# Performance work log

Hardware: AMD Instinct MI355X
Metric: run time of the kernel (lower is better)

## Reference

```python
import jax, jax.numpy as jnp
import numpy as np

NUM_HEADS = 16
HEAD_DIM = 128  # embedding_size 2048 / 16 heads
ROPE_BASE = 10000.0


def rope_tables(seq_len, head_dim):
    # matches precompute_rope_params with freq_config=None
    inv_freq = 1.0 / (ROPE_BASE ** (jnp.arange(0, head_dim, 2, dtype=jnp.float32) / head_dim))
    pos = jnp.arange(seq_len, dtype=jnp.float32)
    ang = pos[:, None] * inv_freq[None, :]          # [S, D/2]
    ang = jnp.concatenate([ang, ang], axis=1)        # [S, D]
    return jnp.cos(ang), jnp.sin(ang)


def apply_rope(x, cos, sin):
    # x: [B, H, S, D]
    d = x.shape[-1]
    x1, x2 = x[..., : d // 2], x[..., d // 2:]
    rotated = jnp.concatenate([-x2, x1], axis=-1)
    return x * cos[None, None] + rotated * sin[None, None]


def setup_inputs() -> dict:
    key = jax.random.key(0)
    ks = jax.random.split(key, 5)
    B, S, H = 2, 2048, 2048
    w_scale = 1.0 / np.sqrt(H)  # keep activations sane
    return {
        "x": jax.random.normal(ks[0], (B, S, H), dtype=jnp.float32),
        "Wq": jax.random.normal(ks[1], (H, H), dtype=jnp.float32) * w_scale,
        "Wk": jax.random.normal(ks[2], (H, H), dtype=jnp.float32) * w_scale,
        "Wv": jax.random.normal(ks[3], (H, H), dtype=jnp.float32) * w_scale,
        "Wo": jax.random.normal(ks[4], (H, H), dtype=jnp.float32) * w_scale,
    }


def reference(x, Wq, Wk, Wv, Wo):
    B, S, H = x.shape
    nH, D = NUM_HEADS, HEAD_DIM
    # torch Linear(bias=False): y = x @ W.T
    q = (x @ Wq.T).reshape(B, S, nH, D).transpose(0, 2, 1, 3)  # [B,H,S,D]
    k = (x @ Wk.T).reshape(B, S, nH, D).transpose(0, 2, 1, 3)
    v = (x @ Wv.T).reshape(B, S, nH, D).transpose(0, 2, 1, 3)
    cos, sin = rope_tables(S, D)
    q = apply_rope(q, cos, sin)
    k = apply_rope(k, cos, sin)  # note: v is NOT rotated, matching source
    # Faithful to source bug: scores / (1/sqrt(d)) == scores * sqrt(d)
    scale = jnp.sqrt(jnp.asarray(D, dtype=x.dtype))
    scores = jnp.einsum("bhqd,bhkd->bhqk", q, k) * scale
    causal = jnp.triu(jnp.ones((S, S), dtype=bool), k=1)
    scores = jnp.where(causal[None, None], -jnp.inf, scores)
    attn = jax.nn.softmax(scores, axis=-1)
    ctx = jnp.einsum("bhqk,bhkd->bhqd", attn, v)
    ctx = ctx.transpose(0, 2, 1, 3).reshape(B, S, H)
    return ctx @ Wo.T
```

## Files before the change

kernel.cpp:

```cpp
#include <hip/hip_runtime.h>
#include <cmath>


typedef unsigned short u16;
typedef __attribute__((ext_vector_type(4))) float  f32x4;
typedef __attribute__((ext_vector_type(16))) float f32x16;
typedef __attribute__((ext_vector_type(4))) float  float4v;
typedef __attribute__((ext_vector_type(4))) unsigned short u16x4;
typedef __attribute__((ext_vector_type(8))) unsigned short u16x8;
typedef __attribute__((ext_vector_type(8))) short s16x8;

__device__ __forceinline__ u16 f2bf(float f) {
  unsigned u = __float_as_uint(f);
  u += 0x7FFFu + ((u >> 16) & 1u);
  return (u16)(u >> 16);
}
__device__ __forceinline__ float bf2f(u16 h) {
  return __uint_as_float(((unsigned)h) << 16);
}
__device__ __forceinline__ f32x4 MFMA(s16x8 a, s16x8 b, f32x4 c) {
  return __builtin_amdgcn_mfma_f32_16x16x32_bf16(a, b, c, 0, 0, 0);
}
__device__ __forceinline__ f32x16 MFMA32(s16x8 a, s16x8 b, f32x16 c) {
  return __builtin_amdgcn_mfma_f32_32x32x16_bf16(a, b, c, 0, 0, 0);
}
__device__ __forceinline__ unsigned cvtpk_bf16(float lo, float hi) {
  unsigned r;
  asm("v_cvt_pk_bf16_f32 %0, %1, %2" : "=v"(r) : "v"(lo), "v"(hi));
  return r;
}
__device__ __forceinline__ void gld16(const void* g, void* s) {
  __builtin_amdgcn_global_load_lds(
      (const __attribute__((address_space(1))) void*)g,
      (__attribute__((address_space(3))) void*)s, 16, 0, 0);
}

__global__ void split_bf16(const float* __restrict__ src, u16* __restrict__ hi,
                           u16* __restrict__ lo, int n4) {
  int i = blockIdx.x * 256 + threadIdx.x;
  if (i >= n4) return;
  float4v v = ((const float4v*)src)[i];
  u16x4 hv, lv;
#pragma unroll
  for (int j = 0; j < 4; ++j) {
    float f = v[j];
    u16 h = f2bf(f);
    hv[j] = h;
    lv[j] = f2bf(f - bf2f(h));
  }
  ((u16x4*)hi)[i] = hv;
  if (lo) ((u16x4*)lo)[i] = lv;
}

__global__ void rope_tab(float* __restrict__ cosT, float* __restrict__ sinT) {
  int idx = blockIdx.x * 256 + threadIdx.x;
  int i = idx & 63, s = idx >> 6;
  double invf = pow(10000.0, -(double)i / 64.0);
  double ang = (double)s * invf;
  cosT[idx] = (float)cos(ang);
  sinT[idx] = (float)sin(ang);
}

template <int NTERM, int OMODE, int ROPE>
__global__ __launch_bounds__(256, 3)
void gemm_bt(const u16* __restrict__ Ah, const u16* __restrict__ Al,
             const u16* __restrict__ Bh, const u16* __restrict__ Bl,
             float* __restrict__ Cf, u16* __restrict__ Ch, u16* __restrict__ Cl,
             const float* __restrict__ cosT, const float* __restrict__ sinT,
             float scale, int M, int N, int K) {
  __shared__ u16 As[128 * 32];
  __shared__ u16 Bs[128 * 32];
  __shared__ u16 Asl[NTERM == 3 ? 128 * 32 : 8];
  __shared__ u16 Bsl[NTERM == 3 ? 128 * 32 : 8];
  const int bn = blockIdx.x, bm = blockIdx.y;
  const int t = threadIdx.x;
  const int w = t >> 6, lane = t & 63, quad = lane >> 4, lc = lane & 15;

  const f32x4 ZERO = {0.f, 0.f, 0.f, 0.f};
  f32x4 acc[2][8];
#pragma unroll
  for (int i = 0; i < 2; ++i)
#pragma unroll
    for (int j = 0; j < 8; ++j) acc[i][j] = ZERO;

  const int sr0 = (lane >> 2);
  const int sc0 = (lane & 3) * 8;
  const size_t arow0 = (size_t)bm * 128, brow0 = (size_t)bn * 128;

  for (int k0 = 0; k0 < K; k0 += 32) {
#pragma unroll
    for (int p = 0; p < 2; ++p) {
      const int ch = 2 * w + p;
      const int r = ch * 16 + sr0;
      const size_t ga = (arow0 + r) * (size_t)K + k0 + sc0;
      const size_t gb = (brow0 + r) * (size_t)K + k0 + sc0;
      const int ldso = ch * 512 + lane * 8;
      gld16(&Ah[ga], &As[ldso]);
      gld16(&Bh[gb], &Bs[ldso]);
      if constexpr (NTERM == 3) {
        gld16(&Al[ga], &Asl[ldso]);
        gld16(&Bl[gb], &Bsl[ldso]);
      }
    }
    __syncthreads();

    s16x8 ah[2], al[2];
#pragma unroll
    for (int i = 0; i < 2; ++i) {
      ah[i] = *(const s16x8*)&As[(32 * w + 16 * i + lc) * 32 + 8 * quad];
      if constexpr (NTERM == 3)
        al[i] = *(const s16x8*)&Asl[(32 * w + 16 * i + lc) * 32 + 8 * quad];
    }
#pragma unroll
    for (int j = 0; j < 8; ++j) {
      const s16x8 bh = *(const s16x8*)&Bs[(16 * j + lc) * 32 + 8 * quad];
      s16x8 bl;
      if constexpr (NTERM == 3)
        bl = *(const s16x8*)&Bsl[(16 * j + lc) * 32 + 8 * quad];
#pragma unroll
      for (int i = 0; i < 2; ++i) {
        acc[i][j] = MFMA(ah[i], bh, acc[i][j]);
        if constexpr (NTERM == 3) {
          acc[i][j] = MFMA(ah[i], bl, acc[i][j]);
          acc[i][j] = MFMA(al[i], bh, acc[i][j]);
        }
      }
    }
    __syncthreads();
  }

  if constexpr (ROPE) {
#pragma unroll
    for (int i = 0; i < 2; ++i)
#pragma unroll
      for (int r = 0; r < 4; ++r) {
        const int row = bm * 128 + 32 * w + 16 * i + 4 * quad + r;
        const int s = row & 2047;
#pragma unroll
        for (int j = 0; j < 4; ++j) {
          const int hd = 16 * j + lc;
          const float cs = cosT[s * 64 + hd], sn = sinT[s * 64 + hd];
          const float q1 = acc[i][j][r], q2 = acc[i][j + 4][r];
          const float o1 = (q1 * cs - q2 * sn) * scale;
          const float o2 = (q2 * cs + q1 * sn) * scale;
          const size_t p1 = (size_t)row * N + bn * 128 + hd;
          const u16 h1 = f2bf(o1);
          Ch[p1] = h1; Cl[p1] = f2bf(o1 - bf2f(h1));
          const u16 h2 = f2bf(o2);
          Ch[p1 + 64] = h2; Cl[p1 + 64] = f2bf(o2 - bf2f(h2));
        }
      }
  } else {
#pragma unroll
    for (int i = 0; i < 2; ++i)
#pragma unroll
      for (int j = 0; j < 8; ++j) {
        const int col = bn * 128 + 16 * j + lc;
#pragma unroll
        for (int r = 0; r < 4; ++r) {
          const int row = bm * 128 + 32 * w + 16 * i + 4 * quad + r;
          const float v = acc[i][j][r];
          if constexpr (OMODE == 0) {
            Cf[(size_t)row * N + col] = v;
          } else if constexpr (OMODE == 1) {
            const u16 hv = f2bf(v);
            Ch[(size_t)row * N + col] = hv;
            Cl[(size_t)row * N + col] = f2bf(v - bf2f(hv));
          } else {
            Ch[(size_t)row * N + col] = f2bf(v);
          }
        }
      }
  }
}

__global__ __launch_bounds__(512, 2)
void attn(const u16* __restrict__ Qh, const u16* __restrict__ Ql,
          const u16* __restrict__ Kh, const u16* __restrict__ Kl,
          const u16* __restrict__ Vt, u16* __restrict__ Ctx) {
  __shared__ u16 SMEM[65536];

  const int t = threadIdx.x;
  const int w = t >> 6, lane = t & 63;
  const int l31 = lane & 31, hi = lane >> 5;
  const int swz = (l31 & 7) << 3;
  const int j = w >> 1, kh = w & 1;

  const int bid = (int)blockIdx.x + 8 * (int)blockIdx.y + 128 * (int)blockIdx.z;
  const int xcd = bid & 7, slot = bid >> 3;
  const int h = xcd * 2 + (slot >> 4);
  const int rem = slot & 15;
  const int qtA = rem & 7, bA = rem >> 3;

  const int offK0 = (8 * w + (lane >> 4)) * 2048 + (((lane & 15) ^ ((lane >> 4) & 7)) * 8);
  const int offK1 = (8 * w + 4 + (lane >> 4)) * 2048 + (((lane & 15) ^ ((4 + (lane >> 4)) & 7)) * 8);
  const int offV0 = (16 * w + (lane >> 3)) * 4096 + (((lane & 7) ^ ((lane >> 3) & 7)) * 8);
  const int offV1 = offV0 + 8 * 4096;

  auto stage = [&](const u16* gK, const u16* gKlo, const u16* gV, int kt, int bp) {
    u16* B = &SMEM[bp * 24576];
    const int ka = kt * 131072;
    const int va = kt * 64;
    gld16(gK + ka + offK0, B + 1024 * w);
    gld16(gK + ka + offK1, B + 1024 * w + 512);
    gld16(gKlo + ka + offK0, B + 8192 + 1024 * w);
    gld16(gKlo + ka + offK1, B + 8192 + 1024 * w + 512);
    gld16(gV + va + offV0, B + 16384 + 1024 * w);
    gld16(gV + va + offV1, B + 16384 + 1024 * w + 512);
  };

  int bufph = 0;
  {
    const u16* gK0 = Kh + ((size_t)(bA * 2048)) * 2048 + h * 128;
    const u16* gL0 = Kl + ((size_t)(bA * 2048)) * 2048 + h * 128;
    const u16* gV0 = Vt + (size_t)(h * 128) * 4096 + bA * 2048;
    stage(gK0, gL0, gV0, 0, 0);
  }

  for (int task = 0; task < 2; ++task) {
    const int qt = task ? 15 - qtA : qtA;
    const int bb = task ? 1 - bA : bA;
    const u16* gK0 = Kh + ((size_t)(bb * 2048)) * 2048 + h * 128;
    const u16* gL0 = Kl + ((size_t)(bb * 2048)) * 2048 + h * 128;
    const u16* gV0 = Vt + (size_t)(h * 128) * 4096 + bb * 2048;
    const int nb = 1 - bb;
    const u16* nK0 = Kh + ((size_t)(nb * 2048)) * 2048 + h * 128;
    const u16* nL0 = Kl + ((size_t)(nb * 2048)) * 2048 + h * 128;
    const u16* nV0 = Vt + (size_t)(h * 128) * 4096 + nb * 2048;

    const int q0 = qt * 128 + 32 * j;
    const int qg = q0 + l31;
    s16x8 qfh[8], qfl[8];
    {
      const size_t qbase = ((size_t)(bb * 2048 + qg)) * 2048 + h * 128 + 8 * hi;
#pragma unroll
      for (int s = 0; s < 8; ++s) {
        qfh[s] = *(const s16x8*)&Qh[qbase + 16 * s];
        qfl[s] = *(const s16x8*)&Ql[qbase + 16 * s];
      }
    }

    float m_run = -3.0e38f, l_run = 0.f;
    f32x16 o[4];
#pragma unroll
    for (int d = 0; d < 4; ++d)
#pragma unroll
      for (int r = 0; r < 16; ++r) o[d][r] = 0.f;

    const int nt = 2 * qt + 2;
    for (int kt = 0; kt < nt; ++kt) {
      bool staged = true;
      if (kt + 1 < nt)      stage(gK0, gL0, gV0, kt + 1, bufph ^ 1);
      else if (task == 0)   stage(nK0, nL0, nV0, 0, bufph ^ 1);
      else                  staged = false;
      if (staged) asm volatile("s_waitcnt vmcnt(6)" ::: "memory");
      else        asm volatile("s_waitcnt vmcnt(0)" ::: "memory");
      __builtin_amdgcn_sched_barrier(0);
      __builtin_amdgcn_s_barrier();
      __builtin_amdgcn_sched_barrier(0);

      const int kb0 = kt * 64 + 32 * kh;
      const bool active = (q0 + 31) >= kb0;
      if (active) {
        const u16* Kb = &SMEM[bufph * 24576];
        const u16* Lb = Kb + 8192;
        const u16* Vb = Kb + 16384;
        f32x16 acc;
#pragma unroll
        for (int r = 0; r < 16; ++r) acc[r] = 0.f;
        __builtin_amdgcn_s_setprio(1);
#pragma unroll
        for (int s = 0; s < 8; ++s) {
          const int col = 16 * s + 8 * hi;
          const s16x8 kha = *(const s16x8*)&Kb[((32 * kh + l31) * 128 + col) ^ swz];
          const s16x8 kla = *(const s16x8*)&Lb[((32 * kh + l31) * 128 + col) ^ swz];
          acc = MFMA32(kha, qfh[s], acc);
          acc = MFMA32(kla, qfh[s], acc);
          acc = MFMA32(kha, qfl[s], acc);
        }
        __builtin_amdgcn_s_setprio(0);

        const bool partial = (kb0 + 31) > q0;
        float mx = -3.0e38f;
#pragma unroll
        for (int r = 0; r < 16; ++r) {
          const int koff = (r & 3) + 8 * (r >> 2) + 4 * hi;
          float v = acc[r];
          if (partial && (kb0 + koff > qg)) v = -3.0e38f;
          acc[r] = v;
          mx = fmaxf(mx, v);
        }
        mx = fmaxf(mx, __shfl_xor(mx, 32));
        const float mn = fmaxf(m_run, mx);
        const float al = __expf(m_run - mn);
        m_run = mn;
        float rs = 0.f;
#pragma unroll
        for (int r = 0; r < 16; ++r) {
          const float e = __expf(acc[r] - mn);
          acc[r] = e;
          rs += e;
        }
        rs += __shfl_xor(rs, 32);
        l_run = l_run * al + rs;
#pragma unroll
        for (int d = 0; d < 4; ++d)
#pragma unroll
          for (int r = 0; r < 16; ++r) o[d][r] *= al;

        s16x8 pb[2];
#pragma unroll
        for (int tt = 0; tt < 2; ++tt) {
          const int q2A = 2 * tt;
          const float e0 = acc[4 * q2A + 0], e1 = acc[4 * q2A + 1];
          const float e2 = acc[4 * q2A + 2], e3 = acc[4 * q2A + 3];
          const float f0 = acc[4 * q2A + 4], f1 = acc[4 * q2A + 5];
          const float f2 = acc[4 * q2A + 6], f3 = acc[4 * q2A + 7];
          unsigned a0 = cvtpk_bf16(e0, e1);
          unsigned a1 = cvtpk_bf16(e2, e3);
          unsigned b0 = cvtpk_bf16(f0, f1);
          unsigned b1 = cvtpk_bf16(f2, f3);
          asm volatile("v_permlane32_swap_b32 %0, %1" : "+v"(a0), "+v"(b0));
          asm volatile("v_permlane32_swap_b32 %0, %1" : "+v"(a1), "+v"(b1));
          union { unsigned u[4]; s16x8 v; } pk;
          pk.u[0] = a0; pk.u[1] = a1; pk.u[2] = b0; pk.u[3] = b1;
          pb[tt] = pk.v;
        }

        __builtin_amdgcn_s_setprio(1);
#pragma unroll
        for (int d = 0; d < 4; ++d) {
#pragma unroll
          for (int tt = 0; tt < 2; ++tt) {
            const s16x8 va = *(const s16x8*)
                &Vb[((32 * d + l31) * 64 + 16 * (2 * kh + tt) + 8 * hi) ^ swz];
            o[d] = MFMA32(va, pb[tt], o[d]);
          }
        }
        __builtin_amdgcn_s_setprio(0);
      }
      __builtin_amdgcn_s_barrier();
      bufph ^= 1;
    }

    float* Sf = (float*)&SMEM[49152];
    Sf[w * 64 + lane] = m_run;
    Sf[512 + w * 64 + lane] = l_run;
    asm volatile("s_waitcnt lgkmcnt(0)" ::: "memory");
    __builtin_amdgcn_s_barrier();
    const float mOth = Sf[(w ^ 1) * 64 + lane];
    const float lOth = Sf[512 + (w ^ 1) * 64 + lane];
    const float mC = fmaxf(m_run, mOth);
    const float eS = __expf(m_run - mC);
    const float eO = __expf(mOth - mC);
    const float lC = eS * l_run + eO * lOth;
#pragma unroll
    for (int d = 0; d < 4; ++d)
#pragma unroll
      for (int r = 0; r < 16; ++r) o[d][r] *= eS;
    __builtin_amdgcn_s_barrier();
#pragma unroll
    for (int round = 0; round < 2; ++round) {
      if ((w >> 2) == round && kh == 1) {
        const int sl = j & 1;
#pragma unroll
        for (int d = 0; d < 4; ++d)
#pragma unroll
          for (int rr = 0; rr < 4; ++rr) {
            float4v c;
            c[0] = o[d][4 * rr + 0]; c[1] = o[d][4 * rr + 1];
            c[2] = o[d][4 * rr + 2]; c[3] = o[d][4 * rr + 3];
            const int cidx = 4 * (d * 4 + rr);
            *(float4v*)&Sf[sl * 4096 + ((lane * 64 + cidx) ^ ((lane & 7) << 2))] = c;
          }
      }
      asm volatile("s_waitcnt lgkmcnt(0)" ::: "memory");
      __builtin_amdgcn_s_barrier();
      if ((w >> 2) == round && kh == 0) {
        const int sl = j & 1;
#pragma unroll
        for (int d = 0; d < 4; ++d)
#pragma unroll
          for (int rr = 0; rr < 4; ++rr) {
            const int cidx = 4 * (d * 4 + rr);
            const float4v c =
                *(const float4v*)&Sf[sl * 4096 + ((lane * 64 + cidx) ^ ((lane & 7) << 2))];
            o[d][4 * rr + 0] += c[0]; o[d][4 * rr + 1] += c[1];
            o[d][4 * rr + 2] += c[2]; o[d][4 * rr + 3] += c[3];
          }
      }
      __builtin_amdgcn_s_barrier();
    }
    u16* Os = &SMEM[49152];
    if (kh == 0) {
      const float inv_l = 1.0f / lC;
      const int rl = 32 * j + l31;
#pragma unroll
      for (int d = 0; d < 4; ++d)
#pragma unroll
        for (int r = 0; r < 16; r += 2) {
          const int dd = 32 * d + (r & 3) + 8 * (r >> 2) + 4 * hi;
          const unsigned pr = cvtpk_bf16(o[d][r] * inv_l, o[d][r + 1] * inv_l);
          *(unsigned*)&Os[(rl * 128 + dd) ^ ((rl & 7) << 3)] = pr;
        }
    }
    asm volatile("s_waitcnt lgkmcnt(0)" ::: "memory");
    __builtin_amdgcn_s_barrier();
    {
      const int rr = t >> 2, cb = (t & 3) * 32;
      const size_t ob =
          ((size_t)(bb * 2048 + qt * 128 + rr)) * 2048 + h * 128 + cb;
#pragma unroll
      for (int p = 0; p < 4; ++p)
        *(u16x8*)&Ctx[ob + 8 * p] =
            *(const u16x8*)&Os[(rr * 128 + cb + 8 * p) ^ ((rr & 7) << 3)];
    }
    asm volatile("s_waitcnt lgkmcnt(0)" ::: "memory");
    __builtin_amdgcn_s_barrier();
  }
}

extern "C" void kernel_launch(void* const* d_in, const int* in_sizes, int n_in,
                              void* d_out, int out_size, void* d_ws, size_t ws_size,
                              hipStream_t stream) {
  const float* x  = (const float*)d_in[0];
  const float* Wq = (const float*)d_in[1];
  const float* Wk = (const float*)d_in[2];
  const float* Wv = (const float*)d_in[3];
  const float* Wo = (const float*)d_in[4];
  float* out = (float*)d_out;

  char* ws = (char*)d_ws;
  size_t off = 0;
  auto alloc = [&](size_t bytes) {
    char* p = ws + off;
    off += (bytes + 255) & ~(size_t)255;
    return p;
  };
  const size_t XE = (size_t)4096 * 2048;
  const size_t WE = (size_t)2048 * 2048;

  u16* xh  = (u16*)alloc(XE * 2);
  u16* xl  = (u16*)alloc(XE * 2);
  u16* Wqh = (u16*)alloc(WE * 2);
  u16* Wql = (u16*)alloc(WE * 2);
  u16* Wkh = (u16*)alloc(WE * 2);
  u16* Wkl = (u16*)alloc(WE * 2);
  u16* Wvh = (u16*)alloc(WE * 2);
  u16* Woh = (u16*)alloc(WE * 2);
  u16* Qhb = (u16*)alloc(XE * 2);
  u16* Qlb = (u16*)alloc(XE * 2);
  u16* Khb = (u16*)alloc(XE * 2);
  u16* Klb = (u16*)alloc(XE * 2);
  u16* Vtb = (u16*)alloc(XE * 2);
  u16* Ctxb = (u16*)alloc(XE * 2);
  float* cosT = (float*)alloc((size_t)2048 * 64 * 4);
  float* sinT = (float*)alloc((size_t)2048 * 64 * 4);
  (void)ws_size;
  (void)in_sizes; (void)n_in; (void)out_size;

  split_bf16<<<8192, 256, 0, stream>>>(x, xh, xl, (int)(XE / 4));
  split_bf16<<<4096, 256, 0, stream>>>(Wq, Wqh, Wql, (int)(WE / 4));
  split_bf16<<<4096, 256, 0, stream>>>(Wk, Wkh, Wkl, (int)(WE / 4));
  split_bf16<<<4096, 256, 0, stream>>>(Wv, Wvh, nullptr, (int)(WE / 4));
  split_bf16<<<4096, 256, 0, stream>>>(Wo, Woh, nullptr, (int)(WE / 4));
  rope_tab<<<512, 256, 0, stream>>>(cosT, sinT);

  gemm_bt<3, 1, 1><<<dim3(16, 32), 256, 0, stream>>>(
      xh, xl, Wqh, Wql, nullptr, Qhb, Qlb, cosT, sinT,
      11.313708498984760f, 4096, 2048, 2048);
  gemm_bt<3, 1, 1><<<dim3(16, 32), 256, 0, stream>>>(
      xh, xl, Wkh, Wkl, nullptr, Khb, Klb, cosT, sinT,
      1.0f, 4096, 2048, 2048);
  gemm_bt<1, 2, 0><<<dim3(32, 16), 256, 0, stream>>>(
      Wvh, nullptr, xh, nullptr, nullptr, Vtb, nullptr, nullptr, nullptr,
      1.0f, 2048, 4096, 2048);

  attn<<<dim3(8, 16, 2), 512, 0, stream>>>(Qhb, Qlb, Khb, Klb, Vtb, Ctxb);

  gemm_bt<1, 0, 0><<<dim3(16, 32), 256, 0, stream>>>(
      Ctxb, nullptr, Woh, nullptr, out, nullptr, nullptr, nullptr, nullptr,
      1.0f, 4096, 2048, 2048);
}
```

Before: 570.5 us.

## Rewrite projection GEMMs with 256x128 tiles, double-buffered LDS and 32x32 MFMA

Measured after the change: 548.9 us. -3.8%, faster.

```diff
diff --git a/kernel.cpp b/kernel.cpp
--- a/kernel.cpp
+++ b/kernel.cpp
@@ -17,9 +17,6 @@
 }
 __device__ __forceinline__ float bf2f(u16 h) {
   return __uint_as_float(((unsigned)h) << 16);
-}
-__device__ __forceinline__ f32x4 MFMA(s16x8 a, s16x8 b, f32x4 c) {
-  return __builtin_amdgcn_mfma_f32_16x16x32_bf16(a, b, c, 0, 0, 0);
 }
 __device__ __forceinline__ f32x16 MFMA32(s16x8 a, s16x8 b, f32x16 c) {
   return __builtin_amdgcn_mfma_f32_32x32x16_bf16(a, b, c, 0, 0, 0);
@@ -62,104 +59,142 @@
 }
 
 template <int NTERM, int OMODE, int ROPE>
-__global__ __launch_bounds__(256, 3)
-void gemm_bt(const u16* __restrict__ Ah, const u16* __restrict__ Al,
-             const u16* __restrict__ Bh, const u16* __restrict__ Bl,
-             float* __restrict__ Cf, u16* __restrict__ Ch, u16* __restrict__ Cl,
-             const float* __restrict__ cosT, const float* __restrict__ sinT,
-             float scale, int M, int N, int K) {
-  __shared__ u16 As[128 * 32];
-  __shared__ u16 Bs[128 * 32];
-  __shared__ u16 Asl[NTERM == 3 ? 128 * 32 : 8];
-  __shared__ u16 Bsl[NTERM == 3 ? 128 * 32 : 8];
+__global__ __launch_bounds__(512, 1)
+void gemm8(const u16* __restrict__ Ah, const u16* __restrict__ Al,
+           const u16* __restrict__ Bh, const u16* __restrict__ Bl,
+           float* __restrict__ Cf, u16* __restrict__ Ch, u16* __restrict__ Cl,
+           const float* __restrict__ cosT, const float* __restrict__ sinT,
+           float scale, int M, int N, int K) {
+  constexpr int BUF = (NTERM == 3) ? 24576 : 12288;
+  constexpr int BHI = (NTERM == 3) ? 16384 : 8192;
+  __shared__ u16 SM[2 * BUF];
   const int bn = blockIdx.x, bm = blockIdx.y;
   const int t = threadIdx.x;
-  const int w = t >> 6, lane = t & 63, quad = lane >> 4, lc = lane & 15;
-
-  const f32x4 ZERO = {0.f, 0.f, 0.f, 0.f};
-  f32x4 acc[2][8];
-#pragma unroll
-  for (int i = 0; i < 2; ++i)
-#pragma unroll
-    for (int j = 0; j < 8; ++j) acc[i][j] = ZERO;
-
-  const int sr0 = (lane >> 2);
-  const int sc0 = (lane & 3) * 8;
-  const size_t arow0 = (size_t)bm * 128, brow0 = (size_t)bn * 128;
-
-  for (int k0 = 0; k0 < K; k0 += 32) {
-#pragma unroll
-    for (int p = 0; p < 2; ++p) {
-      const int ch = 2 * w + p;
-      const int r = ch * 16 + sr0;
-      const size_t ga = (arow0 + r) * (size_t)K + k0 + sc0;
-      const size_t gb = (brow0 + r) * (size_t)K + k0 + sc0;
-      const int ldso = ch * 512 + lane * 8;
-      gld16(&Ah[ga], &As[ldso]);
-      gld16(&Bh[gb], &Bs[ldso]);
-      if constexpr (NTERM == 3) {
-        gld16(&Al[ga], &Asl[ldso]);
-        gld16(&Bl[gb], &Bsl[ldso]);
-      }
-    }
-    __syncthreads();
-
-    s16x8 ah[2], al[2];
-#pragma unroll
-    for (int i = 0; i < 2; ++i) {
-      ah[i] = *(const s16x8*)&As[(32 * w + 16 * i + lc) * 32 + 8 * quad];
+  const int w = t >> 6, lane = t & 63;
+  const int l31 = lane & 31, hi = lane >> 5;
+  const int wm = w >> 1, wn = w & 1;
+
+  const size_t arow0 = (size_t)bm * 256, brow0 = (size_t)bn * 128;
+
+  const int pA0 = 128 * w + lane;
+  const int pA1 = pA0 + 64;
+  const int pB0 = 64 * w + lane;
+  const int qA0 = pA0 ^ ((pA0 >> 3) & 7);
+  const int qA1 = pA1 ^ ((pA1 >> 3) & 7);
+  const int qB0 = pB0 ^ ((pB0 >> 3) & 7);
+  const size_t gA0 = (arow0 + (qA0 >> 2)) * (size_t)K + (qA0 & 3) * 8;
+  const size_t gA1 = (arow0 + (qA1 >> 2)) * (size_t)K + (qA1 & 3) * 8;
+  const size_t gB0 = (brow0 + (qB0 >> 2)) * (size_t)K + (qB0 & 3) * 8;
+
+  auto stage = [&](int k0, int bp) {
+    u16* P = &SM[bp * BUF];
+    gld16(&Ah[gA0 + k0], P + 1024 * w);
+    gld16(&Ah[gA1 + k0], P + 1024 * w + 512);
+    gld16(&Bh[gB0 + k0], P + BHI + 512 * w);
+    if constexpr (NTERM == 3) {
+      gld16(&Al[gA0 + k0], P + 8192 + 1024 * w);
+      gld16(&Al[gA1 + k0], P + 8192 + 1024 * w + 512);
+      gld16(&Bl[gB0 + k0], P + BHI + 4096 + 512 * w);
+    }
+  };
+
+  auto aoff = [&](int fm, int ks) {
+    int q = ((64 * wm + 32 * fm + l31) << 2) | (2 * ks + hi);
+    q ^= (q >> 3) & 7;
+    return q * 8;
+  };
+  auto boff = [&](int fn, int ks) {
+    int q = ((32 * wn + 64 * fn + l31) << 2) | (2 * ks + hi);
+    q ^= (q >> 3) & 7;
+    return q * 8;
+  };
+
+  f32x16 acc[2][2];
+#pragma unroll
+  for (int fm = 0; fm < 2; ++fm)
+#pragma unroll
+    for (int fn = 0; fn < 2; ++fn)
+#pragma unroll
+      for (int r = 0; r < 16; ++r) acc[fm][fn][r] = 0.f;
+
+  stage(0, 0);
+  const int NK = K >> 5;
+  int bp = 0;
+  for (int kt = 0; kt < NK; ++kt) {
+    if (kt + 1 < NK) {
+      stage((kt + 1) * 32, bp ^ 1);
       if constexpr (NTERM == 3)
-        al[i] = *(const s16x8*)&Asl[(32 * w + 16 * i + lc) * 32 + 8 * quad];
-    }
-#pragma unroll
-    for (int j = 0; j < 8; ++j) {
-      const s16x8 bh = *(const s16x8*)&Bs[(16 * j + lc) * 32 + 8 * quad];
-      s16x8 bl;
-      if constexpr (NTERM == 3)
-        bl = *(const s16x8*)&Bsl[(16 * j + lc) * 32 + 8 * quad];
-#pragma unroll
-      for (int i = 0; i < 2; ++i) {
-        acc[i][j] = MFMA(ah[i], bh, acc[i][j]);
-        if constexpr (NTERM == 3) {
-          acc[i][j] = MFMA(ah[i], bl, acc[i][j]);
-          acc[i][j] = MFMA(al[i], bh, acc[i][j]);
-        }
-      }
-    }
-    __syncthreads();
+        asm volatile("s_waitcnt vmcnt(6)" ::: "memory");
+      else
+        asm volatile("s_waitcnt vmcnt(3)" ::: "memory");
+    } else {
+      asm volatile("s_waitcnt vmcnt(0)" ::: "memory");
+    }
+    __builtin_amdgcn_sched_barrier(0);
+    __builtin_amdgcn_s_barrier();
+    __builtin_amdgcn_sched_barrier(0);
+
+    const u16* P = &SM[bp * BUF];
+    __builtin_amdgcn_s_setprio(1);
+#pragma unroll
+    for (int ks = 0; ks < 2; ++ks) {
+      s16x8 a_h[2], a_l[2], b_h[2], b_l[2];
+#pragma unroll
+      for (int fm = 0; fm < 2; ++fm) {
+        a_h[fm] = *(const s16x8*)&P[aoff(fm, ks)];
+        if constexpr (NTERM == 3)
+          a_l[fm] = *(const s16x8*)&P[8192 + aoff(fm, ks)];
+      }
+#pragma unroll
+      for (int fn = 0; fn < 2; ++fn) {
+        b_h[fn] = *(const s16x8*)&P[BHI + boff(fn, ks)];
+        if constexpr (NTERM == 3)
+          b_l[fn] = *(const s16x8*)&P[BHI + 4096 + boff(fn, ks)];
+      }
+#pragma unroll
+      for (int fm = 0; fm < 2; ++fm)
+#pragma unroll
+        for (int fn = 0; fn < 2; ++fn) {
+          acc[fm][fn] = MFMA32(a_h[fm], b_h[fn], acc[fm][fn]);
+          if constexpr (NTERM == 3) {
+            acc[fm][fn] = MFMA32(a_h[fm], b_l[fn], acc[fm][fn]);
+            acc[fm][fn] = MFMA32(a_l[fm], b_h[fn], acc[fm][fn]);
+          }
+        }
+    }
+    __builtin_amdgcn_s_setprio(0);
+    __builtin_amdgcn_s_barrier();
+    bp ^= 1;
   }
 
   if constexpr (ROPE) {
-#pragma unroll
-    for (int i = 0; i < 2; ++i)
-#pragma unroll
-      for (int r = 0; r < 4; ++r) {
-        const int row = bm * 128 + 32 * w + 16 * i + 4 * quad + r;
+    const int hd = 32 * wn + l31;
+#pragma unroll
+    for (int fm = 0; fm < 2; ++fm)
+#pragma unroll
+      for (int r = 0; r < 16; ++r) {
+        const int row = bm * 256 + 64 * wm + 32 * fm + (r & 3) + 8 * (r >> 2) + 4 * hi;
         const int s = row & 2047;
-#pragma unroll
-        for (int j = 0; j < 4; ++j) {
-          const int hd = 16 * j + lc;
-          const float cs = cosT[s * 64 + hd], sn = sinT[s * 64 + hd];
-          const float q1 = acc[i][j][r], q2 = acc[i][j + 4][r];
-          const float o1 = (q1 * cs - q2 * sn) * scale;
-          const float o2 = (q2 * cs + q1 * sn) * scale;
-          const size_t p1 = (size_t)row * N + bn * 128 + hd;
-          const u16 h1 = f2bf(o1);
-          Ch[p1] = h1; Cl[p1] = f2bf(o1 - bf2f(h1));
-          const u16 h2 = f2bf(o2);
-          Ch[p1 + 64] = h2; Cl[p1 + 64] = f2bf(o2 - bf2f(h2));
-        }
+        const float cs = cosT[s * 64 + hd], sn = sinT[s * 64 + hd];
+        const float q1 = acc[fm][0][r], q2 = acc[fm][1][r];
+        const float o1 = (q1 * cs - q2 * sn) * scale;
+        const float o2 = (q2 * cs + q1 * sn) * scale;
+        const size_t p1 = (size_t)row * N + bn * 128 + hd;
+        const u16 h1 = f2bf(o1);
+        Ch[p1] = h1; Cl[p1] = f2bf(o1 - bf2f(h1));
+        const u16 h2 = f2bf(o2);
+        Ch[p1 + 64] = h2; Cl[p1 + 64] = f2bf(o2 - bf2f(h2));
       }
   } else {
 #pragma unroll
-    for (int i = 0; i < 2; ++i)
-#pragma unroll
-      for (int j = 0; j < 8; ++j) {
-        const int col = bn * 128 + 16 * j + lc;
-#pragma unroll
-        for (int r = 0; r < 4; ++r) {
-          const int row = bm * 128 + 32 * w + 16 * i + 4 * quad + r;
-          const float v = acc[i][j][r];
+    for (int fm = 0; fm < 2; ++fm)
+#pragma unroll
+      for (int fn = 0; fn < 2; ++fn)
+#pragma unroll
+        for (int r = 0; r < 16; ++r) {
+          const int row = bm * 256 + 64 * wm + 32 * fm + (r & 3) + 8 * (r >> 2) + 4 * hi;
+          const int col = bn * 128 + 32 * wn + 64 * fn + l31;
+          const float v = acc[fm][fn][r];
           if constexpr (OMODE == 0) {
             Cf[(size_t)row * N + col] = v;
           } else if constexpr (OMODE == 1) {
@@ -170,7 +205,6 @@
             Ch[(size_t)row * N + col] = f2bf(v);
           }
         }
-      }
   }
 }
 
@@ -466,19 +500,19 @@
   split_bf16<<<4096, 256, 0, stream>>>(Wo, Woh, nullptr, (int)(WE / 4));
   rope_tab<<<512, 256, 0, stream>>>(cosT, sinT);
 
-  gemm_bt<3, 1, 1><<<dim3(16, 32), 256, 0, stream>>>(
+  gemm8<3, 1, 1><<<dim3(16, 16), 512, 0, stream>>>(
       xh, xl, Wqh, Wql, nullptr, Qhb, Qlb, cosT, sinT,
       11.313708498984760f, 4096, 2048, 2048);
-  gemm_bt<3, 1, 1><<<dim3(16, 32), 256, 0, stream>>>(
+  gemm8<3, 1, 1><<<dim3(16, 16), 512, 0, stream>>>(
       xh, xl, Wkh, Wkl, nullptr, Khb, Klb, cosT, sinT,
       1.0f, 4096, 2048, 2048);
-  gemm_bt<1, 2, 0><<<dim3(32, 16), 256, 0, stream>>>(
+  gemm8<1, 2, 0><<<dim3(32, 8), 512, 0, stream>>>(
       Wvh, nullptr, xh, nullptr, nullptr, Vtb, nullptr, nullptr, nullptr,
       1.0f, 2048, 4096, 2048);
 
   attn<<<dim3(8, 16, 2), 512, 0, stream>>>(Qhb, Qlb, Khb, Klb, Vtb, Ctxb);
 
-  gemm_bt<1, 0, 0><<<dim3(16, 32), 256, 0, stream>>>(
+  gemm8<1, 0, 0><<<dim3(16, 16), 512, 0, stream>>>(
       Ctxb, nullptr, Woh, nullptr, out, nullptr, nullptr, nullptr, nullptr,
       1.0f, 4096, 2048, 2048);
 }
```
